# Kernel optimization log

Hardware: AMD Instinct MI355X
Metric: run time of the kernel (lower is better)

The kernel has to match this reference:

```python
import jax, jax.numpy as jnp
import numpy as np

B, T, V, E, U = 1024, 128, 32000, 128, 512


def setup_inputs() -> dict:
    key = jax.random.key(0)
    ks = jax.random.split(key, 8)
    s = lambda k, *sh: jax.random.normal(k, sh, dtype=jnp.float32) * 0.05
    return {
        "tokens": jax.random.randint(ks[0], (B, T), 0, V, dtype=jnp.int32),
        "emb": s(ks[1], V, E),
        "Wx0": s(ks[2], E, U),
        "Wh0": s(ks[3], U, U),
        "b0": jnp.zeros((U,), jnp.float32),
        "Wx1": s(ks[4], U, U),
        "Wh1": s(ks[5], U, U),
        "b1": jnp.zeros((U,), jnp.float32),
        "Wo": s(ks[6], U, 1),
        "bo": jnp.zeros((1,), jnp.float32),
    }


def reference(tokens, emb, Wx0, Wh0, b0, Wx1, Wh1, b1, Wo, bo):
    # Embedding lookup: [B, T, E]
    x = emb[tokens]
    xs = jnp.swapaxes(x, 0, 1)  # [T, B, E] for time-major scan
    h0 = jnp.zeros((tokens.shape[0], Wh0.shape[0]), x.dtype)
    h1 = jnp.zeros((tokens.shape[0], Wh1.shape[0]), x.dtype)

    def step(carry, xt):
        h0, h1 = carry
        # SimpleRNNCell layer 0: h' = tanh(x@Wx + h@Wh + b)
        h0 = jnp.tanh(xt @ Wx0 + h0 @ Wh0 + b0)
        # SimpleRNNCell layer 1 stacked on out0
        h1 = jnp.tanh(h0 @ Wx1 + h1 @ Wh1 + b1)
        return (h0, h1), None

    (h0, h1), _ = jax.lax.scan(step, (h0, h1), xs)
    logits = h1 @ Wo + bo            # [B, 1]
    return jax.nn.sigmoid(logits)
```

## Files before the change

kernel.cpp:

```cpp
#include <hip/hip_runtime.h>
#include <hip/hip_bf16.h>

#define B_ 1024
#define T_ 128
#define E_ 128
#define U_ 512
#define V_ 32000
#define NC 16
#define NG 16
#define MB 64
#define NB 32

#define CTR_OFF 0
#define H0H_OFF (1u << 20)
#define H0L_OFF (3u << 20)
#define H1H_OFF (5u << 20)
#define H1L_OFF (7u << 20)
#define EMBW_OFF (9u << 20)
#define ZERO_BYTES (9u << 20)

typedef unsigned int uint32;
typedef __bf16 bf16x8 __attribute__((ext_vector_type(8)));
typedef float f32x4 __attribute__((ext_vector_type(4)));
typedef unsigned short us8 __attribute__((ext_vector_type(8)));

__device__ __forceinline__ unsigned short f2b(float f) {
  uint32 u = __builtin_bit_cast(uint32, f);
  u += 0x7fffu + ((u >> 16) & 1u);
  return (unsigned short)(u >> 16);
}
__device__ __forceinline__ float b2f(unsigned short h) {
  return __builtin_bit_cast(float, (uint32)h << 16);
}

__device__ __forceinline__ bf16x8 lds_frag(const unsigned short* s, int row, int k, int K) {
  uint32 off = (uint32)((row * K + k) * 2) ^ (uint32)((row & 7) << 4);
  us8 v = *(const us8*)((const char*)s + off);
  return __builtin_bit_cast(bf16x8, v);
}
__device__ __forceinline__ bf16x8 g_frag(const unsigned short* p) {
  us8 v = *(const us8*)p;
  return __builtin_bit_cast(bf16x8, v);
}
__device__ __forceinline__ void st_coh(unsigned short* p, unsigned short v) {
  __hip_atomic_store(p, v, __ATOMIC_RELAXED, __HIP_MEMORY_SCOPE_AGENT);
}

__device__ __forceinline__ void groupbar(uint32* ctr, int phase, int g, int tid) {
  asm volatile("s_waitcnt vmcnt(0)" ::: "memory");
  __syncthreads();
  if (tid == 0) {
    uint32* a = &ctr[(uint32)((phase << 4) | g) << 4];
    __hip_atomic_fetch_add(a, 1u, __ATOMIC_RELAXED, __HIP_MEMORY_SCOPE_AGENT);
    while (__hip_atomic_load(a, __ATOMIC_RELAXED, __HIP_MEMORY_SCOPE_AGENT) < NC)
      __builtin_amdgcn_s_sleep(1);
    __builtin_amdgcn_fence(__ATOMIC_ACQUIRE, "agent");
  }
  __syncthreads();
}

__global__ void rnn_init(unsigned char* ws) {
  const uint4 z = {0u, 0u, 0u, 0u};
  uint4* p = (uint4*)ws;
  size_t n = ZERO_BYTES / 16;
  for (size_t j = (size_t)blockIdx.x * blockDim.x + threadIdx.x; j < n;
       j += (size_t)gridDim.x * blockDim.x)
    p[j] = z;
}

__global__ __launch_bounds__(256) void embw_gemm(const float* __restrict__ emb,
                                                 const float* __restrict__ Wx0,
                                                 unsigned short* __restrict__ embW) {
  const int tid = threadIdx.x;
  const int lane = tid & 63;
  const int wv = tid >> 6;
  const int arow = lane & 15;
  const int kgrp = (lane >> 4) * 8;
  const int vrow = blockIdx.x * 64 + wv * 16;

  bf16x8 a[4];
  for (int kt = 0; kt < 4; ++kt) {
    const float* p = emb + (size_t)(vrow + arow) * E_ + kt * 32 + kgrp;
    float4 f0 = ((const float4*)p)[0];
    float4 f1 = ((const float4*)p)[1];
    us8 u;
    u[0] = f2b(f0.x); u[1] = f2b(f0.y); u[2] = f2b(f0.z); u[3] = f2b(f0.w);
    u[4] = f2b(f1.x); u[5] = f2b(f1.y); u[6] = f2b(f1.z); u[7] = f2b(f1.w);
    a[kt] = __builtin_bit_cast(bf16x8, u);
  }
  const int c0 = blockIdx.y * 64;
  for (int nt = 0; nt < 4; ++nt) {
    const int col = c0 + nt * 16 + (lane & 15);
    f32x4 acc = {0.f, 0.f, 0.f, 0.f};
    for (int kt = 0; kt < 4; ++kt) {
      us8 ub;
      for (int j = 0; j < 8; ++j)
        ub[j] = f2b(Wx0[(size_t)(kt * 32 + kgrp + j) * U_ + col]);
      acc = __builtin_amdgcn_mfma_f32_16x16x32_bf16(a[kt], __builtin_bit_cast(bf16x8, ub),
                                                    acc, 0, 0, 0);
    }
    const int crow = vrow + (lane >> 4) * 4;
    for (int i = 0; i < 4; ++i)
      embW[(size_t)(crow + i) * U_ + col] = f2b(acc[i]);
  }
}

__global__ __launch_bounds__(512, 2) void rnn_main(
    const int* __restrict__ tokens, const float* __restrict__ b0,
    const float* __restrict__ Wh0, const float* __restrict__ Wx1,
    const float* __restrict__ Wh1, const float* __restrict__ b1,
    unsigned char* ws) {
  __shared__ unsigned short sWh0h[NB * U_];
  __shared__ unsigned short sWh0l[NB * U_];
  __shared__ unsigned short sWx1h[NB * U_];
  __shared__ unsigned short sWh1h[NB * U_];
  __shared__ unsigned short sWh1l[NB * 480];

  const int tid = threadIdx.x;
  const int bid = blockIdx.x;
  const int g = bid & (NG - 1);
  const int c = bid >> 4;
  const int r0 = g * MB;
  const int c0 = c * NB;

  uint32* ctr = (uint32*)(ws + CTR_OFF);
  unsigned short* h0h = (unsigned short*)(ws + H0H_OFF);
  unsigned short* h0l = (unsigned short*)(ws + H0L_OFF);
  unsigned short* h1h = (unsigned short*)(ws + H1H_OFF);
  unsigned short* h1l = (unsigned short*)(ws + H1L_OFF);
  const unsigned short* embW = (const unsigned short*)(ws + EMBW_OFF);

  for (int idx = tid; idx < NB * U_; idx += 512) {
    int cl = idx & 31, k = idx >> 5;
    float v = Wh0[(size_t)k * U_ + c0 + cl];
    unsigned short hi = f2b(v);
    uint32 off = (uint32)((cl * U_ + k) * 2) ^ (uint32)((cl & 7) << 4);
    *(unsigned short*)((char*)sWh0h + off) = hi;
    *(unsigned short*)((char*)sWh0l + off) = f2b(v - b2f(hi));
  }
  for (int idx = tid; idx < NB * U_; idx += 512) {
    int cl = idx & 31, k = idx >> 5;
    float v = Wx1[(size_t)k * U_ + c0 + cl];
    uint32 off = (uint32)((cl * U_ + k) * 2) ^ (uint32)((cl & 7) << 4);
    *(unsigned short*)((char*)sWx1h + off) = f2b(v);
  }
  for (int idx = tid; idx < NB * U_; idx += 512) {
    int cl = idx & 31, k = idx >> 5;
    float v = Wh1[(size_t)k * U_ + c0 + cl];
    unsigned short hi = f2b(v);
    uint32 off = (uint32)((cl * U_ + k) * 2) ^ (uint32)((cl & 7) << 4);
    *(unsigned short*)((char*)sWh1h + off) = hi;
    if (k < 480) {
      uint32 offl = (uint32)((cl * 480 + k) * 2) ^ (uint32)((cl & 7) << 4);
      *(unsigned short*)((char*)sWh1l + offl) = f2b(v - b2f(hi));
    }
  }

  const int lane = tid & 63;
  const int wv = tid >> 6;
  const int mt = wv >> 1;
  const int nt = wv & 1;
  const int colL = nt * 16 + (lane & 15);
  const int rowB = mt * 16 + ((lane >> 4) << 2);
  const int arow = lane & 15;
  const int kgrp = (lane >> 4) * 8;
  const int rowA = r0 + mt * 16 + arow;
  const float b0v = b0[c0 + colL];
  const float b1v = b1[c0 + colL];

  __syncthreads();

  unsigned short embPre[4];
  {
    for (int i = 0; i < 4; ++i) {
      int tk = tokens[(size_t)(r0 + rowB + i) * T_ + 0];
      embPre[i] = embW[(size_t)tk * U_ + c0 + colL];
    }
  }

  for (int t = 0; t <= T_; ++t) {
    const size_t rb0 = (size_t)((t & 1) ^ 1) * (B_ * U_);

    bf16x8 h0h_r[16], h0l_r[16];
    {
      const unsigned short* aph = h0h + rb0 + (size_t)rowA * U_ + kgrp;
      const unsigned short* apl = h0l + rb0 + (size_t)rowA * U_ + kgrp;
#pragma unroll
      for (int kt = 0; kt < 16; ++kt) {
        h0h_r[kt] = g_frag(aph + kt * 32);
        h0l_r[kt] = g_frag(apl + kt * 32);
      }
    }

    if (t >= 1) {
      const size_t rb1 = (size_t)(t & 1) * (B_ * U_);
      const size_t wb1 = (size_t)((t - 1) & 1) * (B_ * U_);
      f32x4 acc = {b1v, b1v, b1v, b1v};
      const unsigned short* a1h = h1h + rb1 + (size_t)rowA * U_ + kgrp;
      const unsigned short* a1l = h1l + rb1 + (size_t)rowA * U_ + kgrp;
#pragma unroll
      for (int kt = 0; kt < 16; ++kt) {
        bf16x8 ah = g_frag(a1h + kt * 32);
        bf16x8 al = g_frag(a1l + kt * 32);
        bf16x8 bxh = lds_frag(sWx1h, colL, kt * 32 + kgrp, U_);
        bf16x8 bh = lds_frag(sWh1h, colL, kt * 32 + kgrp, U_);
        acc = __builtin_amdgcn_mfma_f32_16x16x32_bf16(h0h_r[kt], bxh, acc, 0, 0, 0);
        acc = __builtin_amdgcn_mfma_f32_16x16x32_bf16(h0l_r[kt], bxh, acc, 0, 0, 0);
        acc = __builtin_amdgcn_mfma_f32_16x16x32_bf16(ah, bh, acc, 0, 0, 0);
        acc = __builtin_amdgcn_mfma_f32_16x16x32_bf16(al, bh, acc, 0, 0, 0);
        if (kt < 15) {
          bf16x8 bl = lds_frag(sWh1l, colL, kt * 32 + kgrp, 480);
          acc = __builtin_amdgcn_mfma_f32_16x16x32_bf16(ah, bl, acc, 0, 0, 0);
        }
      }
      size_t ob = wb1 + (size_t)(r0 + rowB) * U_ + (c0 + colL);
      for (int i = 0; i < 4; ++i) {
        float v = tanhf(acc[i]);
        unsigned short hi = f2b(v);
        st_coh(&h1h[ob + (size_t)i * U_], hi);
        st_coh(&h1l[ob + (size_t)i * U_], f2b(v - b2f(hi)));
      }
    }

    if (t < T_) {
      const size_t wbuf = (size_t)(t & 1) * (B_ * U_);
      f32x4 acc;
      for (int i = 0; i < 4; ++i) acc[i] = b0v + b2f(embPre[i]);
#pragma unroll
      for (int kt = 0; kt < 16; ++kt) {
        bf16x8 bh = lds_frag(sWh0h, colL, kt * 32 + kgrp, U_);
        bf16x8 bl = lds_frag(sWh0l, colL, kt * 32 + kgrp, U_);
        acc = __builtin_amdgcn_mfma_f32_16x16x32_bf16(h0h_r[kt], bh, acc, 0, 0, 0);
        acc = __builtin_amdgcn_mfma_f32_16x16x32_bf16(h0l_r[kt], bh, acc, 0, 0, 0);
        acc = __builtin_amdgcn_mfma_f32_16x16x32_bf16(h0h_r[kt], bl, acc, 0, 0, 0);
      }
      size_t ob = wbuf + (size_t)(r0 + rowB) * U_ + (c0 + colL);
      for (int i = 0; i < 4; ++i) {
        float v = tanhf(acc[i]);
        unsigned short hi = f2b(v);
        st_coh(&h0h[ob + (size_t)i * U_], hi);
        st_coh(&h0l[ob + (size_t)i * U_], f2b(v - b2f(hi)));
      }

      if (t + 1 < T_) {
        for (int i = 0; i < 4; ++i) {
          int tk = tokens[(size_t)(r0 + rowB + i) * T_ + (t + 1)];
          embPre[i] = embW[(size_t)tk * U_ + c0 + colL];
        }
      }
      groupbar(ctr, t, g, tid);
    }
  }
}

__global__ void rnn_final(const unsigned short* __restrict__ h1h,
                          const unsigned short* __restrict__ h1l,
                          const float* __restrict__ Wo,
                          const float* __restrict__ bo, float* __restrict__ out) {
  int lane = threadIdx.x & 63;
  int b = blockIdx.x * 4 + (threadIdx.x >> 6);
  us8 hh = *(const us8*)(h1h + (size_t)b * U_ + lane * 8);
  us8 hl = *(const us8*)(h1l + (size_t)b * U_ + lane * 8);
  const float4* wp = (const float4*)(Wo + lane * 8);
  float4 w0 = wp[0], w1 = wp[1];
  float s = (b2f(hh[0]) + b2f(hl[0])) * w0.x + (b2f(hh[1]) + b2f(hl[1])) * w0.y +
            (b2f(hh[2]) + b2f(hl[2])) * w0.z + (b2f(hh[3]) + b2f(hl[3])) * w0.w +
            (b2f(hh[4]) + b2f(hl[4])) * w1.x + (b2f(hh[5]) + b2f(hl[5])) * w1.y +
            (b2f(hh[6]) + b2f(hl[6])) * w1.z + (b2f(hh[7]) + b2f(hl[7])) * w1.w;
  for (int off = 32; off > 0; off >>= 1) s += __shfl_down(s, off, 64);
  if (lane == 0) out[b] = 1.0f / (1.0f + expf(-(s + bo[0])));
}

extern "C" void kernel_launch(void* const* d_in, const int* in_sizes, int n_in,
                              void* d_out, int out_size, void* d_ws, size_t ws_size,
                              hipStream_t stream) {
  const int* tokens = (const int*)d_in[0];
  const float* emb = (const float*)d_in[1];
  const float* Wx0 = (const float*)d_in[2];
  const float* Wh0 = (const float*)d_in[3];
  const float* b0 = (const float*)d_in[4];
  const float* Wx1 = (const float*)d_in[5];
  const float* Wh1 = (const float*)d_in[6];
  const float* b1 = (const float*)d_in[7];
  const float* Wo = (const float*)d_in[8];
  const float* bo = (const float*)d_in[9];
  unsigned char* ws = (unsigned char*)d_ws;
  float* out = (float*)d_out;

  hipLaunchKernelGGL(rnn_init, dim3(1024), dim3(256), 0, stream, ws);
  hipLaunchKernelGGL(embw_gemm, dim3(V_ / 64, U_ / 64), dim3(256), 0, stream,
                     emb, Wx0, (unsigned short*)(ws + EMBW_OFF));
  hipLaunchKernelGGL(rnn_main, dim3(NC * NG), dim3(512), 0, stream, tokens,
                     b0, Wh0, Wx1, Wh1, b1, ws);
  hipLaunchKernelGGL(rnn_final, dim3(256), dim3(256), 0, stream,
                     (const unsigned short*)(ws + H1H_OFF) + (size_t)1 * B_ * U_,
                     (const unsigned short*)(ws + H1L_OFF) + (size_t)1 * B_ * U_,
                     Wo, bo, out);
}
```

Baseline: 2.393 ms.

## Use cheaper non-coherent stores and L1 invalidate when group shares one XCD

At startup each block records its XCD id in a per-group bitmask, then a group barrier checks whether all 16 blocks of a row group sit on the same XCD. If they do, the time loop switches to plain stores for hidden states, and the barrier replaces the agent-scope acquire fence with a buffer_inv L1 invalidate, avoiding slower coherent stores and fence cost. Otherwise the original coherent path runs. The XCD placement depends on the dispatch order, so the fast path may never trigger; if it does, correctness relies on shared L2 within one XCD.

After: 2.225 ms. 1.08x faster.

```diff
diff --git a/kernel.cpp b/kernel.cpp
--- a/kernel.cpp
+++ b/kernel.cpp
@@ -12,6 +12,7 @@
 #define NB 32
 
 #define CTR_OFF 0
+#define XMASK_OFF (512u << 10)
 #define H0H_OFF (1u << 20)
 #define H0L_OFF (3u << 20)
 #define H1H_OFF (5u << 20)
@@ -45,8 +46,13 @@
 __device__ __forceinline__ void st_coh(unsigned short* p, unsigned short v) {
   __hip_atomic_store(p, v, __ATOMIC_RELAXED, __HIP_MEMORY_SCOPE_AGENT);
 }
-
-__device__ __forceinline__ void groupbar(uint32* ctr, int phase, int g, int tid) {
+template <bool FAST>
+__device__ __forceinline__ void st_h(unsigned short* p, unsigned short v) {
+  if (FAST) *p = v; else st_coh(p, v);
+}
+
+__device__ __forceinline__ void bar_core(uint32* ctr, int phase, int g, int tid,
+                                         bool fence, bool l1inv) {
   asm volatile("s_waitcnt vmcnt(0)" ::: "memory");
   __syncthreads();
   if (tid == 0) {
@@ -54,7 +60,8 @@
     __hip_atomic_fetch_add(a, 1u, __ATOMIC_RELAXED, __HIP_MEMORY_SCOPE_AGENT);
     while (__hip_atomic_load(a, __ATOMIC_RELAXED, __HIP_MEMORY_SCOPE_AGENT) < NC)
       __builtin_amdgcn_s_sleep(1);
-    __builtin_amdgcn_fence(__ATOMIC_ACQUIRE, "agent");
+    if (fence) __builtin_amdgcn_fence(__ATOMIC_ACQUIRE, "agent");
+    if (l1inv) asm volatile("buffer_inv" ::: "memory");
   }
   __syncthreads();
 }
@@ -105,77 +112,18 @@
   }
 }
 
-__global__ __launch_bounds__(512, 2) void rnn_main(
-    const int* __restrict__ tokens, const float* __restrict__ b0,
-    const float* __restrict__ Wh0, const float* __restrict__ Wx1,
-    const float* __restrict__ Wh1, const float* __restrict__ b1,
-    unsigned char* ws) {
-  __shared__ unsigned short sWh0h[NB * U_];
-  __shared__ unsigned short sWh0l[NB * U_];
-  __shared__ unsigned short sWx1h[NB * U_];
-  __shared__ unsigned short sWh1h[NB * U_];
-  __shared__ unsigned short sWh1l[NB * 480];
-
-  const int tid = threadIdx.x;
-  const int bid = blockIdx.x;
-  const int g = bid & (NG - 1);
-  const int c = bid >> 4;
-  const int r0 = g * MB;
-  const int c0 = c * NB;
-
-  uint32* ctr = (uint32*)(ws + CTR_OFF);
-  unsigned short* h0h = (unsigned short*)(ws + H0H_OFF);
-  unsigned short* h0l = (unsigned short*)(ws + H0L_OFF);
-  unsigned short* h1h = (unsigned short*)(ws + H1H_OFF);
-  unsigned short* h1l = (unsigned short*)(ws + H1L_OFF);
-  const unsigned short* embW = (const unsigned short*)(ws + EMBW_OFF);
-
-  for (int idx = tid; idx < NB * U_; idx += 512) {
-    int cl = idx & 31, k = idx >> 5;
-    float v = Wh0[(size_t)k * U_ + c0 + cl];
-    unsigned short hi = f2b(v);
-    uint32 off = (uint32)((cl * U_ + k) * 2) ^ (uint32)((cl & 7) << 4);
-    *(unsigned short*)((char*)sWh0h + off) = hi;
-    *(unsigned short*)((char*)sWh0l + off) = f2b(v - b2f(hi));
-  }
-  for (int idx = tid; idx < NB * U_; idx += 512) {
-    int cl = idx & 31, k = idx >> 5;
-    float v = Wx1[(size_t)k * U_ + c0 + cl];
-    uint32 off = (uint32)((cl * U_ + k) * 2) ^ (uint32)((cl & 7) << 4);
-    *(unsigned short*)((char*)sWx1h + off) = f2b(v);
-  }
-  for (int idx = tid; idx < NB * U_; idx += 512) {
-    int cl = idx & 31, k = idx >> 5;
-    float v = Wh1[(size_t)k * U_ + c0 + cl];
-    unsigned short hi = f2b(v);
-    uint32 off = (uint32)((cl * U_ + k) * 2) ^ (uint32)((cl & 7) << 4);
-    *(unsigned short*)((char*)sWh1h + off) = hi;
-    if (k < 480) {
-      uint32 offl = (uint32)((cl * 480 + k) * 2) ^ (uint32)((cl & 7) << 4);
-      *(unsigned short*)((char*)sWh1l + offl) = f2b(v - b2f(hi));
-    }
-  }
-
-  const int lane = tid & 63;
-  const int wv = tid >> 6;
-  const int mt = wv >> 1;
-  const int nt = wv & 1;
-  const int colL = nt * 16 + (lane & 15);
-  const int rowB = mt * 16 + ((lane >> 4) << 2);
-  const int arow = lane & 15;
-  const int kgrp = (lane >> 4) * 8;
-  const int rowA = r0 + mt * 16 + arow;
-  const float b0v = b0[c0 + colL];
-  const float b1v = b1[c0 + colL];
-
-  __syncthreads();
-
+template <bool FAST>
+__device__ __forceinline__ void rnn_loop(
+    const int* __restrict__ tokens, const unsigned short* __restrict__ embW,
+    unsigned short* h0h, unsigned short* h0l, unsigned short* h1h,
+    unsigned short* h1l, uint32* ctr, const unsigned short* sWh0h,
+    const unsigned short* sWh0l, const unsigned short* sWx1h,
+    const unsigned short* sWh1h, const unsigned short* sWh1l, int g, int tid,
+    int r0, int c0, int colL, int rowB, int kgrp, int rowA, float b0v, float b1v) {
   unsigned short embPre[4];
-  {
-    for (int i = 0; i < 4; ++i) {
-      int tk = tokens[(size_t)(r0 + rowB + i) * T_ + 0];
-      embPre[i] = embW[(size_t)tk * U_ + c0 + colL];
-    }
+  for (int i = 0; i < 4; ++i) {
+    int tk = tokens[(size_t)(r0 + rowB + i) * T_ + 0];
+    embPre[i] = embW[(size_t)tk * U_ + c0 + colL];
   }
 
   for (int t = 0; t <= T_; ++t) {
@@ -217,8 +165,8 @@
       for (int i = 0; i < 4; ++i) {
         float v = tanhf(acc[i]);
         unsigned short hi = f2b(v);
-        st_coh(&h1h[ob + (size_t)i * U_], hi);
-        st_coh(&h1l[ob + (size_t)i * U_], f2b(v - b2f(hi)));
+        st_h<FAST>(&h1h[ob + (size_t)i * U_], hi);
+        st_h<FAST>(&h1l[ob + (size_t)i * U_], f2b(v - b2f(hi)));
       }
     }
 
@@ -238,8 +186,8 @@
       for (int i = 0; i < 4; ++i) {
         float v = tanhf(acc[i]);
         unsigned short hi = f2b(v);
-        st_coh(&h0h[ob + (size_t)i * U_], hi);
-        st_coh(&h0l[ob + (size_t)i * U_], f2b(v - b2f(hi)));
+        st_h<FAST>(&h0h[ob + (size_t)i * U_], hi);
+        st_h<FAST>(&h0l[ob + (size_t)i * U_], f2b(v - b2f(hi)));
       }
 
       if (t + 1 < T_) {
@@ -248,9 +196,97 @@
           embPre[i] = embW[(size_t)tk * U_ + c0 + colL];
         }
       }
-      groupbar(ctr, t, g, tid);
-    }
-  }
+      bar_core(ctr, t, g, tid, !FAST, FAST);
+    }
+  }
+}
+
+__global__ __launch_bounds__(512, 2) void rnn_main(
+    const int* __restrict__ tokens, const float* __restrict__ b0,
+    const float* __restrict__ Wh0, const float* __restrict__ Wx1,
+    const float* __restrict__ Wh1, const float* __restrict__ b1,
+    unsigned char* ws) {
+  __shared__ unsigned short sWh0h[NB * U_];
+  __shared__ unsigned short sWh0l[NB * U_];
+  __shared__ unsigned short sWx1h[NB * U_];
+  __shared__ unsigned short sWh1h[NB * U_];
+  __shared__ unsigned short sWh1l[NB * 480];
+  __shared__ uint32 sFast;
+
+  const int tid = threadIdx.x;
+  const int bid = blockIdx.x;
+  const int g = bid & (NG - 1);
+  const int c = bid >> 4;
+  const int r0 = g * MB;
+  const int c0 = c * NB;
+
+  uint32* ctr = (uint32*)(ws + CTR_OFF);
+  unsigned short* h0h = (unsigned short*)(ws + H0H_OFF);
+  unsigned short* h0l = (unsigned short*)(ws + H0L_OFF);
+  unsigned short* h1h = (unsigned short*)(ws + H1H_OFF);
+  unsigned short* h1l = (unsigned short*)(ws + H1L_OFF);
+  const unsigned short* embW = (const unsigned short*)(ws + EMBW_OFF);
+
+  for (int idx = tid; idx < NB * U_; idx += 512) {
+    int cl = idx & 31, k = idx >> 5;
+    float v = Wh0[(size_t)k * U_ + c0 + cl];
+    unsigned short hi = f2b(v);
+    uint32 off = (uint32)((cl * U_ + k) * 2) ^ (uint32)((cl & 7) << 4);
+    *(unsigned short*)((char*)sWh0h + off) = hi;
+    *(unsigned short*)((char*)sWh0l + off) = f2b(v - b2f(hi));
+  }
+  for (int idx = tid; idx < NB * U_; idx += 512) {
+    int cl = idx & 31, k = idx >> 5;
+    float v = Wx1[(size_t)k * U_ + c0 + cl];
+    uint32 off = (uint32)((cl * U_ + k) * 2) ^ (uint32)((cl & 7) << 4);
+    *(unsigned short*)((char*)sWx1h + off) = f2b(v);
+  }
+  for (int idx = tid; idx < NB * U_; idx += 512) {
+    int cl = idx & 31, k = idx >> 5;
+    float v = Wh1[(size_t)k * U_ + c0 + cl];
+    unsigned short hi = f2b(v);
+    uint32 off = (uint32)((cl * U_ + k) * 2) ^ (uint32)((cl & 7) << 4);
+    *(unsigned short*)((char*)sWh1h + off) = hi;
+    if (k < 480) {
+      uint32 offl = (uint32)((cl * 480 + k) * 2) ^ (uint32)((cl & 7) << 4);
+      *(unsigned short*)((char*)sWh1l + offl) = f2b(v - b2f(hi));
+    }
+  }
+
+  {
+    uint32 xcd;
+    asm volatile("s_getreg_b32 %0, hwreg(HW_REG_XCC_ID)" : "=s"(xcd));
+    uint32* xm = (uint32*)(ws + XMASK_OFF) + (uint32)g * 16;
+    if (tid == 0)
+      __hip_atomic_fetch_or(xm, 1u << (xcd & 31u), __ATOMIC_RELAXED,
+                            __HIP_MEMORY_SCOPE_AGENT);
+    bar_core(ctr, T_, g, tid, true, false);
+    if (tid == 0) {
+      uint32 m = __hip_atomic_load(xm, __ATOMIC_RELAXED, __HIP_MEMORY_SCOPE_AGENT);
+      sFast = (__popc(m) == 1) ? 1u : 0u;
+    }
+  }
+
+  const int lane = tid & 63;
+  const int wv = tid >> 6;
+  const int mt = wv >> 1;
+  const int nt = wv & 1;
+  const int colL = nt * 16 + (lane & 15);
+  const int rowB = mt * 16 + ((lane >> 4) << 2);
+  const int kgrp = (lane >> 4) * 8;
+  const int rowA = r0 + mt * 16 + (lane & 15);
+  const float b0v = b0[c0 + colL];
+  const float b1v = b1[c0 + colL];
+
+  __syncthreads();
+  const bool fast = (sFast != 0);
+
+  if (fast)
+    rnn_loop<true>(tokens, embW, h0h, h0l, h1h, h1l, ctr, sWh0h, sWh0l, sWx1h,
+                   sWh1h, sWh1l, g, tid, r0, c0, colL, rowB, kgrp, rowA, b0v, b1v);
+  else
+    rnn_loop<false>(tokens, embW, h0h, h0l, h1h, h1l, ctr, sWh0h, sWh0l, sWx1h,
+                    sWh1h, sWh1l, g, tid, r0, c0, colL, rowB, kgrp, rowA, b0v, b1v);
 }
 
 __global__ void rnn_final(const unsigned short* __restrict__ h1h,
```

## Replace persistent group-barrier kernel with per-timestep launches and pre-transposed global weights

Applied to the files above, without the earlier changes.

The persistent kernel, which synchronised row groups through atomic counter barriers, is replaced by 129 separate rnn_step launches, so kernel boundaries now provide the cross-block synchronisation. Weights are pre-split into bf16 hi/lo parts and transposed into global memory by a new wt_prep kernel, and each step reads them from global/L2 instead of staging them in shared memory. Block-to-tile mapping is reshuffled, and the layer-0 accumulation is split across two accumulators to shorten the MFMA dependency chain. The cost is per-launch overhead and reloading all weights and hidden state from L2 on every step.

After: 4.493 ms. 87.7% more time.

```diff
diff --git a/kernel.cpp b/kernel.cpp
--- a/kernel.cpp
+++ b/kernel.cpp
@@ -10,20 +10,25 @@
 #define NG 16
 #define MB 64
 #define NB 32
-
-#define CTR_OFF 0
-#define H0H_OFF (1u << 20)
-#define H0L_OFF (3u << 20)
-#define H1H_OFF (5u << 20)
-#define H1L_OFF (7u << 20)
-#define EMBW_OFF (9u << 20)
-#define ZERO_BYTES (9u << 20)
+#define HS ((size_t)B_ * U_)
+
+#define H0H_OFF (0u << 20)
+#define H0L_OFF (2u << 20)
+#define H1H_OFF (4u << 20)
+#define H1L_OFF (6u << 20)
+#define WT_OFF (8u << 20)
+#define EMBW_OFF (11u << 20)
+#define ZERO_BYTES (8u << 20)
+
+#define WSZ ((size_t)U_ * U_)
 
 typedef unsigned int uint32;
 typedef __bf16 bf16x8 __attribute__((ext_vector_type(8)));
 typedef float f32x4 __attribute__((ext_vector_type(4)));
 typedef unsigned short us8 __attribute__((ext_vector_type(8)));
 
+#define MFMA __builtin_amdgcn_mfma_f32_16x16x32_bf16
+
 __device__ __forceinline__ unsigned short f2b(float f) {
   uint32 u = __builtin_bit_cast(uint32, f);
   u += 0x7fffu + ((u >> 16) & 1u);
@@ -32,31 +37,9 @@
 __device__ __forceinline__ float b2f(unsigned short h) {
   return __builtin_bit_cast(float, (uint32)h << 16);
 }
-
-__device__ __forceinline__ bf16x8 lds_frag(const unsigned short* s, int row, int k, int K) {
-  uint32 off = (uint32)((row * K + k) * 2) ^ (uint32)((row & 7) << 4);
-  us8 v = *(const us8*)((const char*)s + off);
-  return __builtin_bit_cast(bf16x8, v);
-}
 __device__ __forceinline__ bf16x8 g_frag(const unsigned short* p) {
   us8 v = *(const us8*)p;
   return __builtin_bit_cast(bf16x8, v);
-}
-__device__ __forceinline__ void st_coh(unsigned short* p, unsigned short v) {
-  __hip_atomic_store(p, v, __ATOMIC_RELAXED, __HIP_MEMORY_SCOPE_AGENT);
-}
-
-__device__ __forceinline__ void groupbar(uint32* ctr, int phase, int g, int tid) {
-  asm volatile("s_waitcnt vmcnt(0)" ::: "memory");
-  __syncthreads();
-  if (tid == 0) {
-    uint32* a = &ctr[(uint32)((phase << 4) | g) << 4];
-    __hip_atomic_fetch_add(a, 1u, __ATOMIC_RELAXED, __HIP_MEMORY_SCOPE_AGENT);
-    while (__hip_atomic_load(a, __ATOMIC_RELAXED, __HIP_MEMORY_SCOPE_AGENT) < NC)
-      __builtin_amdgcn_s_sleep(1);
-    __builtin_amdgcn_fence(__ATOMIC_ACQUIRE, "agent");
-  }
-  __syncthreads();
 }
 
 __global__ void rnn_init(unsigned char* ws) {
@@ -66,6 +49,36 @@
   for (size_t j = (size_t)blockIdx.x * blockDim.x + threadIdx.x; j < n;
        j += (size_t)gridDim.x * blockDim.x)
     p[j] = z;
+}
+
+__global__ __launch_bounds__(256) void wt_prep(const float* __restrict__ Wh0,
+                                               const float* __restrict__ Wx1,
+                                               const float* __restrict__ Wh1,
+                                               unsigned char* ws) {
+  unsigned short* Wh0hT = (unsigned short*)(ws + WT_OFF);
+  unsigned short* Wh0lT = Wh0hT + WSZ;
+  unsigned short* Wx1hT = Wh0hT + 2 * WSZ;
+  unsigned short* Wh1hT = Wh0hT + 3 * WSZ;
+  unsigned short* Wh1lT = Wh0hT + 4 * WSZ;
+  size_t idx = (size_t)blockIdx.x * blockDim.x + threadIdx.x;
+  if (idx >= WSZ) return;
+  int k = (int)(idx & (U_ - 1));
+  int col = (int)(idx >> 9);
+  size_t src = (size_t)k * U_ + col;
+  size_t dst = (size_t)col * U_ + k;
+  {
+    float v = Wh0[src];
+    unsigned short hi = f2b(v);
+    Wh0hT[dst] = hi;
+    Wh0lT[dst] = f2b(v - b2f(hi));
+  }
+  Wx1hT[dst] = f2b(Wx1[src]);
+  {
+    float v = Wh1[src];
+    unsigned short hi = f2b(v);
+    Wh1hT[dst] = hi;
+    Wh1lT[dst] = f2b(v - b2f(hi));
+  }
 }
 
 __global__ __launch_bounds__(256) void embw_gemm(const float* __restrict__ emb,
@@ -96,8 +109,7 @@
       us8 ub;
       for (int j = 0; j < 8; ++j)
         ub[j] = f2b(Wx0[(size_t)(kt * 32 + kgrp + j) * U_ + col]);
-      acc = __builtin_amdgcn_mfma_f32_16x16x32_bf16(a[kt], __builtin_bit_cast(bf16x8, ub),
-                                                    acc, 0, 0, 0);
+      acc = MFMA(a[kt], __builtin_bit_cast(bf16x8, ub), acc, 0, 0, 0);
     }
     const int crow = vrow + (lane >> 4) * 4;
     for (int i = 0; i < 4; ++i)
@@ -105,150 +117,111 @@
   }
 }
 
-__global__ __launch_bounds__(512, 2) void rnn_main(
-    const int* __restrict__ tokens, const float* __restrict__ b0,
-    const float* __restrict__ Wh0, const float* __restrict__ Wx1,
-    const float* __restrict__ Wh1, const float* __restrict__ b1,
-    unsigned char* ws) {
-  __shared__ unsigned short sWh0h[NB * U_];
-  __shared__ unsigned short sWh0l[NB * U_];
-  __shared__ unsigned short sWx1h[NB * U_];
-  __shared__ unsigned short sWh1h[NB * U_];
-  __shared__ unsigned short sWh1l[NB * 480];
-
-  const int tid = threadIdx.x;
+__global__ __launch_bounds__(512) void rnn_step(
+    int t, const int* __restrict__ tokens, const float* __restrict__ b0,
+    const float* __restrict__ b1, unsigned char* ws) {
   const int bid = blockIdx.x;
-  const int g = bid & (NG - 1);
-  const int c = bid >> 4;
+  const int xslot = bid & 7;
+  const int j = bid >> 3;
+  const int c = xslot * 2 + (j & 1);
+  const int g = j >> 1;
   const int r0 = g * MB;
   const int c0 = c * NB;
 
-  uint32* ctr = (uint32*)(ws + CTR_OFF);
   unsigned short* h0h = (unsigned short*)(ws + H0H_OFF);
   unsigned short* h0l = (unsigned short*)(ws + H0L_OFF);
   unsigned short* h1h = (unsigned short*)(ws + H1H_OFF);
   unsigned short* h1l = (unsigned short*)(ws + H1L_OFF);
+  const unsigned short* Wh0hT = (const unsigned short*)(ws + WT_OFF);
+  const unsigned short* Wh0lT = Wh0hT + WSZ;
+  const unsigned short* Wx1hT = Wh0hT + 2 * WSZ;
+  const unsigned short* Wh1hT = Wh0hT + 3 * WSZ;
+  const unsigned short* Wh1lT = Wh0hT + 4 * WSZ;
   const unsigned short* embW = (const unsigned short*)(ws + EMBW_OFF);
 
-  for (int idx = tid; idx < NB * U_; idx += 512) {
-    int cl = idx & 31, k = idx >> 5;
-    float v = Wh0[(size_t)k * U_ + c0 + cl];
-    unsigned short hi = f2b(v);
-    uint32 off = (uint32)((cl * U_ + k) * 2) ^ (uint32)((cl & 7) << 4);
-    *(unsigned short*)((char*)sWh0h + off) = hi;
-    *(unsigned short*)((char*)sWh0l + off) = f2b(v - b2f(hi));
-  }
-  for (int idx = tid; idx < NB * U_; idx += 512) {
-    int cl = idx & 31, k = idx >> 5;
-    float v = Wx1[(size_t)k * U_ + c0 + cl];
-    uint32 off = (uint32)((cl * U_ + k) * 2) ^ (uint32)((cl & 7) << 4);
-    *(unsigned short*)((char*)sWx1h + off) = f2b(v);
-  }
-  for (int idx = tid; idx < NB * U_; idx += 512) {
-    int cl = idx & 31, k = idx >> 5;
-    float v = Wh1[(size_t)k * U_ + c0 + cl];
-    unsigned short hi = f2b(v);
-    uint32 off = (uint32)((cl * U_ + k) * 2) ^ (uint32)((cl & 7) << 4);
-    *(unsigned short*)((char*)sWh1h + off) = hi;
-    if (k < 480) {
-      uint32 offl = (uint32)((cl * 480 + k) * 2) ^ (uint32)((cl & 7) << 4);
-      *(unsigned short*)((char*)sWh1l + offl) = f2b(v - b2f(hi));
-    }
-  }
-
+  const int tid = threadIdx.x;
   const int lane = tid & 63;
   const int wv = tid >> 6;
   const int mt = wv >> 1;
   const int nt = wv & 1;
-  const int colL = nt * 16 + (lane & 15);
+  const int l15 = lane & 15;
+  const int colL = nt * 16 + l15;
+  const int colG = c0 + colL;
   const int rowB = mt * 16 + ((lane >> 4) << 2);
-  const int arow = lane & 15;
   const int kgrp = (lane >> 4) * 8;
-  const int rowA = r0 + mt * 16 + arow;
-  const float b0v = b0[c0 + colL];
-  const float b1v = b1[c0 + colL];
-
-  __syncthreads();
-
-  unsigned short embPre[4];
+  const int rowA = r0 + mt * 16 + l15;
+
+  const size_t rb0 = (size_t)((t & 1) ^ 1) * HS;
+
+  bf16x8 h0h_r[16], h0l_r[16];
   {
+    const unsigned short* aph = h0h + rb0 + (size_t)rowA * U_ + kgrp;
+    const unsigned short* apl = h0l + rb0 + (size_t)rowA * U_ + kgrp;
+#pragma unroll
+    for (int kt = 0; kt < 16; ++kt) {
+      h0h_r[kt] = g_frag(aph + kt * 32);
+      h0l_r[kt] = g_frag(apl + kt * 32);
+    }
+  }
+
+  if (t >= 1) {
+    const float b1v = b1[colG];
+    const size_t rb1 = (size_t)(t & 1) * HS;
+    const size_t wb1 = (size_t)((t - 1) & 1) * HS;
+    f32x4 acc = {b1v, b1v, b1v, b1v};
+    const unsigned short* a1h = h1h + rb1 + (size_t)rowA * U_ + kgrp;
+    const unsigned short* a1l = h1l + rb1 + (size_t)rowA * U_ + kgrp;
+    const unsigned short* wx = Wx1hT + (size_t)colG * U_ + kgrp;
+    const unsigned short* wh = Wh1hT + (size_t)colG * U_ + kgrp;
+    const unsigned short* wl = Wh1lT + (size_t)colG * U_ + kgrp;
+#pragma unroll
+    for (int kt = 0; kt < 16; ++kt) {
+      bf16x8 ah = g_frag(a1h + kt * 32);
+      bf16x8 bxh = g_frag(wx + kt * 32);
+      bf16x8 bh = g_frag(wh + kt * 32);
+      acc = MFMA(h0h_r[kt], bxh, acc, 0, 0, 0);
+      acc = MFMA(h0l_r[kt], bxh, acc, 0, 0, 0);
+      bf16x8 al = g_frag(a1l + kt * 32);
+      acc = MFMA(ah, bh, acc, 0, 0, 0);
+      acc = MFMA(al, bh, acc, 0, 0, 0);
+      if (kt < 15) {
+        bf16x8 bl = g_frag(wl + kt * 32);
+        acc = MFMA(ah, bl, acc, 0, 0, 0);
+      }
+    }
+    size_t ob = wb1 + (size_t)(r0 + rowB) * U_ + colG;
     for (int i = 0; i < 4; ++i) {
-      int tk = tokens[(size_t)(r0 + rowB + i) * T_ + 0];
-      embPre[i] = embW[(size_t)tk * U_ + c0 + colL];
-    }
-  }
-
-  for (int t = 0; t <= T_; ++t) {
-    const size_t rb0 = (size_t)((t & 1) ^ 1) * (B_ * U_);
-
-    bf16x8 h0h_r[16], h0l_r[16];
-    {
-      const unsigned short* aph = h0h + rb0 + (size_t)rowA * U_ + kgrp;
-      const unsigned short* apl = h0l + rb0 + (size_t)rowA * U_ + kgrp;
+      float v = tanhf(acc[i]);
+      unsigned short hi = f2b(v);
+      h1h[ob + (size_t)i * U_] = hi;
+      h1l[ob + (size_t)i * U_] = f2b(v - b2f(hi));
+    }
+  }
+
+  if (t < T_) {
+    const float b0v = b0[colG];
+    const size_t wbuf = (size_t)(t & 1) * HS;
+    f32x4 aC, aD = {0.f, 0.f, 0.f, 0.f};
+    for (int i = 0; i < 4; ++i) {
+      int tk = tokens[(size_t)(r0 + rowB + i) * T_ + t];
+      aC[i] = b0v + b2f(embW[(size_t)tk * U_ + colG]);
+    }
+    const unsigned short* wh = Wh0hT + (size_t)colG * U_ + kgrp;
+    const unsigned short* wl = Wh0lT + (size_t)colG * U_ + kgrp;
 #pragma unroll
-      for (int kt = 0; kt < 16; ++kt) {
-        h0h_r[kt] = g_frag(aph + kt * 32);
-        h0l_r[kt] = g_frag(apl + kt * 32);
-      }
-    }
-
-    if (t >= 1) {
-      const size_t rb1 = (size_t)(t & 1) * (B_ * U_);
-      const size_t wb1 = (size_t)((t - 1) & 1) * (B_ * U_);
-      f32x4 acc = {b1v, b1v, b1v, b1v};
-      const unsigned short* a1h = h1h + rb1 + (size_t)rowA * U_ + kgrp;
-      const unsigned short* a1l = h1l + rb1 + (size_t)rowA * U_ + kgrp;
-#pragma unroll
-      for (int kt = 0; kt < 16; ++kt) {
-        bf16x8 ah = g_frag(a1h + kt * 32);
-        bf16x8 al = g_frag(a1l + kt * 32);
-        bf16x8 bxh = lds_frag(sWx1h, colL, kt * 32 + kgrp, U_);
-        bf16x8 bh = lds_frag(sWh1h, colL, kt * 32 + kgrp, U_);
-        acc = __builtin_amdgcn_mfma_f32_16x16x32_bf16(h0h_r[kt], bxh, acc, 0, 0, 0);
-        acc = __builtin_amdgcn_mfma_f32_16x16x32_bf16(h0l_r[kt], bxh, acc, 0, 0, 0);
-        acc = __builtin_amdgcn_mfma_f32_16x16x32_bf16(ah, bh, acc, 0, 0, 0);
-        acc = __builtin_amdgcn_mfma_f32_16x16x32_bf16(al, bh, acc, 0, 0, 0);
-        if (kt < 15) {
-          bf16x8 bl = lds_frag(sWh1l, colL, kt * 32 + kgrp, 480);
-          acc = __builtin_amdgcn_mfma_f32_16x16x32_bf16(ah, bl, acc, 0, 0, 0);
-        }
-      }
-      size_t ob = wb1 + (size_t)(r0 + rowB) * U_ + (c0 + colL);
-      for (int i = 0; i < 4; ++i) {
-        float v = tanhf(acc[i]);
-        unsigned short hi = f2b(v);
-        st_coh(&h1h[ob + (size_t)i * U_], hi);
-        st_coh(&h1l[ob + (size_t)i * U_], f2b(v - b2f(hi)));
-      }
-    }
-
-    if (t < T_) {
-      const size_t wbuf = (size_t)(t & 1) * (B_ * U_);
-      f32x4 acc;
-      for (int i = 0; i < 4; ++i) acc[i] = b0v + b2f(embPre[i]);
-#pragma unroll
-      for (int kt = 0; kt < 16; ++kt) {
-        bf16x8 bh = lds_frag(sWh0h, colL, kt * 32 + kgrp, U_);
-        bf16x8 bl = lds_frag(sWh0l, colL, kt * 32 + kgrp, U_);
-        acc = __builtin_amdgcn_mfma_f32_16x16x32_bf16(h0h_r[kt], bh, acc, 0, 0, 0);
-        acc = __builtin_amdgcn_mfma_f32_16x16x32_bf16(h0l_r[kt], bh, acc, 0, 0, 0);
-        acc = __builtin_amdgcn_mfma_f32_16x16x32_bf16(h0h_r[kt], bl, acc, 0, 0, 0);
-      }
-      size_t ob = wbuf + (size_t)(r0 + rowB) * U_ + (c0 + colL);
-      for (int i = 0; i < 4; ++i) {
-        float v = tanhf(acc[i]);
-        unsigned short hi = f2b(v);
-        st_coh(&h0h[ob + (size_t)i * U_], hi);
-        st_coh(&h0l[ob + (size_t)i * U_], f2b(v - b2f(hi)));
-      }
-
-      if (t + 1 < T_) {
-        for (int i = 0; i < 4; ++i) {
-          int tk = tokens[(size_t)(r0 + rowB + i) * T_ + (t + 1)];
-          embPre[i] = embW[(size_t)tk * U_ + c0 + colL];
-        }
-      }
-      groupbar(ctr, t, g, tid);
+    for (int kt = 0; kt < 16; ++kt) {
+      bf16x8 bh = g_frag(wh + kt * 32);
+      bf16x8 bl = g_frag(wl + kt * 32);
+      aC = MFMA(h0h_r[kt], bh, aC, 0, 0, 0);
+      aD = MFMA(h0l_r[kt], bh, aD, 0, 0, 0);
+      aD = MFMA(h0h_r[kt], bl, aD, 0, 0, 0);
+    }
+    size_t ob = wbuf + (size_t)(r0 + rowB) * U_ + colG;
+    for (int i = 0; i < 4; ++i) {
+      float v = tanhf(aC[i] + aD[i]);
+      unsigned short hi = f2b(v);
+      h0h[ob + (size_t)i * U_] = hi;
+      h0l[ob + (size_t)i * U_] = f2b(v - b2f(hi));
     }
   }
 }
@@ -288,10 +261,14 @@
   float* out = (float*)d_out;
 
   hipLaunchKernelGGL(rnn_init, dim3(1024), dim3(256), 0, stream, ws);
+  hipLaunchKernelGGL(wt_prep, dim3((U_ * U_ + 255) / 256), dim3(256), 0, stream,
+                     Wh0, Wx1, Wh1, ws);
   hipLaunchKernelGGL(embw_gemm, dim3(V_ / 64, U_ / 64), dim3(256), 0, stream,
                      emb, Wx0, (unsigned short*)(ws + EMBW_OFF));
-  hipLaunchKernelGGL(rnn_main, dim3(NC * NG), dim3(512), 0, stream, tokens,
-                     b0, Wh0, Wx1, Wh1, b1, ws);
+  for (int t = 0; t <= T_; ++t) {
+    hipLaunchKernelGGL(rnn_step, dim3(NC * NG), dim3(512), 0, stream, t,
+                       tokens, b0, b1, ws);
+  }
   hipLaunchKernelGGL(rnn_final, dim3(256), dim3(256), 0, stream,
                      (const unsigned short*)(ws + H1H_OFF) + (size_t)1 * B_ * U_,
                      (const unsigned short*)(ws + H1L_OFF) + (size_t)1 * B_ * U_,
```
